# Kernel tuning notes

Measured on AMD Instinct MI355X. Metric: run time of the kernel, lower is better.

## Reference

```python
import jax, jax.numpy as jnp
import numpy as np

B, S, M, H, P, T = 32, 400, 400, 200, 16, 4

def setup_inputs() -> dict:
    key = jax.random.key(0)
    ks = jax.random.split(key, 20)
    sc = 0.05
    inp = {
        'att': jax.random.normal(ks[0], (B, S, M), jnp.float32),
        'mod': jax.random.normal(ks[1], (B, S, M), jnp.float32),
        'mask': jnp.ones((B, S), jnp.float32),
        # LSTMCell: input 2*M, hidden H, gate order i,f,g,o
        'lstm_Wih': jax.random.normal(ks[2], (4 * H, 2 * M), jnp.float32) * sc,
        'lstm_Whh': jax.random.normal(ks[3], (4 * H, H), jnp.float32) * sc,
        'lstm_bih': jnp.zeros((4 * H,), jnp.float32),
        'lstm_bhh': jnp.zeros((4 * H,), jnp.float32),
    }
    for pfx, off in (('s', 4), ('e', 11)):
        inp[pfx + '_rW'] = jax.random.normal(ks[off + 0], (H, 2 * M + H), jnp.float32) * sc
        inp[pfx + '_W1'] = jax.random.normal(ks[off + 1], (P * H, M + H), jnp.float32) * sc
        inp[pfx + '_b1'] = jnp.zeros((P * H,), jnp.float32)
        inp[pfx + '_W2'] = jax.random.normal(ks[off + 2], (P * H, H), jnp.float32) * sc
        inp[pfx + '_b2'] = jnp.zeros((P * H,), jnp.float32)
        inp[pfx + '_W3'] = jax.random.normal(ks[off + 3], (P, 2 * H), jnp.float32) * sc
        inp[pfx + '_b3'] = jnp.zeros((P,), jnp.float32)
    return inp

def _gather(mod, idx):
    # mod:[B,S,M], idx:[B] -> [B,M]
    return jnp.take_along_axis(mod, idx[:, None, None], axis=1)[:, 0, :]

def _lstm_cell(x, h, c, Wih, Whh, bih, bhh):
    g = x @ Wih.T + bih + h @ Whh.T + bhh  # [B,4H]
    i, f, gg, o = jnp.split(g, 4, axis=1)
    c2 = jax.nn.sigmoid(f) * c + jax.nn.sigmoid(i) * jnp.tanh(gg)
    h2 = jax.nn.sigmoid(o) * jnp.tanh(c2)
    return h2, c2

def _hmn(mod, h, us, ue, mask, rW, W1, b1, W2, b2, W3, b3):
    r = jnp.tanh(jnp.concatenate([h, us, ue], 1) @ rW.T)  # [B,H]
    x = jnp.concatenate([mod, jnp.broadcast_to(r[:, None, :], (B, S, H))], 2)  # [B,S,M+H]
    m1 = (x @ W1.T + b1).reshape(B, S, P, H).max(2)   # maxout 1
    m2 = (m1 @ W2.T + b2).reshape(B, S, P, H).max(2)  # maxout 2
    logits = (jnp.concatenate([m1, m2], 2) @ W3.T + b3).max(2)  # [B,S]
    logits = jnp.where(mask > 0, logits, -1e30)
    return jax.nn.log_softmax(logits, axis=1)

def reference(att, mod, mask, lstm_Wih, lstm_Whh, lstm_bih, lstm_bhh,
              s_rW, s_W1, s_b1, s_W2, s_b2, s_W3, s_b3,
              e_rW, e_W1, e_b1, e_W2, e_b2, e_W3, e_b3):
    s_prev = jnp.zeros((B,), jnp.int32)
    e_prev = jnp.sum(mask, 1).astype(jnp.int32) - 1
    h = jnp.zeros((B, H), mod.dtype)
    c = jnp.zeros((B, H), mod.dtype)
    log_p1s, log_p2s = [], []
    for _ in range(T):
        u_s = _gather(mod, s_prev)
        u_e = _gather(mod, e_prev)
        h, c = _lstm_cell(jnp.concatenate([u_s, u_e], 1), h, c,
                          lstm_Wih, lstm_Whh, lstm_bih, lstm_bhh)
        lp1 = _hmn(mod, h, u_s, u_e, mask, s_rW, s_W1, s_b1, s_W2, s_b2, s_W3, s_b3)
        s_prev = jnp.argmax(lp1, axis=1).astype(jnp.int32)
        u_s = _gather(mod, s_prev)
        lp2 = _hmn(mod, h, u_s, u_e, mask, e_rW, e_W1, e_b1, e_W2, e_b2, e_W3, e_b3)
        e_prev = jnp.argmax(lp2, axis=1).astype(jnp.int32)
        log_p1s.append(lp1)
        log_p2s.append(lp2)
    return jnp.stack(log_p1s, 1), jnp.stack(log_p2s, 1)  # each [B,T,S]
```

## Files before the change

kernel.cpp:

```cpp
#include <hip/hip_runtime.h>
#include <math.h>

#define NB 32
#define NS 400
#define NM 400
#define NH 200
#define NP 16
#define NT 4
#define NBS (NB*NS)
#define NPH (NP*NH)
#define NX  (2*NM)
#define NG  (4*NH)
#define NR  (2*NM+NH)
#define K1  1280
#define K2  640

typedef __attribute__((ext_vector_type(8))) short short8v;
typedef __attribute__((ext_vector_type(4))) float f32x4;
typedef __attribute__((ext_vector_type(4))) unsigned short us4;
typedef unsigned short ushort;

__device__ __forceinline__ float sigf(float x){ return 1.0f/(1.0f+expf(-x)); }

__device__ __forceinline__ ushort f2bf(float x){
  union{float f; unsigned u;} v; v.f=x;
  unsigned r = v.u + 0x7fffu + ((v.u>>16)&1u);
  return (ushort)(r>>16);
}
__device__ __forceinline__ float bf2f(ushort u){
  union{float f; unsigned v;} x; x.v = ((unsigned)u)<<16; return x.f;
}
__device__ __forceinline__ float wave_sum(float v){
  #pragma unroll
  for (int o=32;o>0;o>>=1) v += __shfl_xor(v, o);
  return v;
}

__global__ __launch_bounds__(256) void init_kernel(const float* __restrict__ mask,
    float* __restrict__ h, float* __restrict__ c,
    int* __restrict__ sprev, int* __restrict__ eprev){
  int b = blockIdx.x, tid = threadIdx.x;
  __shared__ float red[256];
  float s = 0.f;
  for (int i=tid;i<NS;i+=256) s += mask[(size_t)b*NS+i];
  red[tid]=s; __syncthreads();
  for (int st=128;st>0;st>>=1){ if(tid<st) red[tid]+=red[tid+st]; __syncthreads(); }
  if (tid==0){ sprev[b]=0; eprev[b]=(int)red[0]-1; }
  for (int i=tid;i<NH;i+=256){ h[(size_t)b*NH+i]=0.f; c[(size_t)b*NH+i]=0.f; }
}

__global__ __launch_bounds__(256) void conv_mod_k(const float* __restrict__ in, ushort* __restrict__ out){
  for (size_t i = (size_t)blockIdx.x*256+threadIdx.x; i < (size_t)NBS*NM; i += (size_t)gridDim.x*256){
    int r = (int)(i/NM), k = (int)(i%NM);
    float x = in[i];
    ushort h = f2bf(x); ushort lo = f2bf(x - bf2f(h));
    ushort* o = out + (size_t)r*K1;
    o[k]=h; o[NM+k]=lo; o[2*NM+k]=h;
  }
}
__global__ __launch_bounds__(256) void conv_w1_k(const float* __restrict__ in, ushort* __restrict__ out){
  for (size_t i = (size_t)blockIdx.x*256+threadIdx.x; i < (size_t)NPH*NM; i += (size_t)gridDim.x*256){
    int j = (int)(i/NM), k = (int)(i%NM);
    int jp = (j%NH)*NP + j/NH;
    float x = in[(size_t)j*(NM+NH)+k];
    ushort h = f2bf(x); ushort lo = f2bf(x - bf2f(h));
    ushort* o = out + (size_t)jp*K1;
    o[k]=h; o[NM+k]=h; o[2*NM+k]=lo;
  }
}
__global__ __launch_bounds__(256) void conv_w2_k(const float* __restrict__ in, ushort* __restrict__ out){
  for (size_t i = (size_t)blockIdx.x*256+threadIdx.x; i < (size_t)NPH*NH; i += (size_t)gridDim.x*256){
    int j = (int)(i/NH), k = (int)(i%NH);
    int jp = (j%NH)*NP + j/NH;
    float x = in[(size_t)j*NH+k];
    ushort h = f2bf(x); ushort lo = f2bf(x - bf2f(h));
    ushort* o = out + (size_t)jp*K2;
    o[k]=h; o[NH+k]=h; o[2*NH+k]=lo;
  }
}
__global__ __launch_bounds__(256) void conv_w1r_k(const float* __restrict__ in, float* __restrict__ out){
  for (size_t i = (size_t)blockIdx.x*256+threadIdx.x; i < (size_t)NH*NPH; i += (size_t)gridDim.x*256){
    int k = (int)(i/NPH), jp = (int)(i%NPH);
    int hh = jp>>4, p = jp&15, j = p*NH + hh;
    out[i] = in[(size_t)j*(NM+NH) + NM + k];
  }
}
__global__ __launch_bounds__(256) void permv_k(const float* __restrict__ in, float* __restrict__ out){
  int i = blockIdx.x*256+threadIdx.x;
  if (i < NPH) out[(i%NH)*NP + i/NH] = in[i];
}
__global__ __launch_bounds__(256) void pad_zero_k(ushort* __restrict__ p, int stride, int start, int width, int rows){
  for (size_t i = (size_t)blockIdx.x*256+threadIdx.x; i < (size_t)rows*width; i += (size_t)gridDim.x*256){
    int r = (int)(i/width), j = (int)(i%width);
    p[(size_t)r*stride + start + j] = 0;
  }
}

__global__ __launch_bounds__(256) void lstm_gates(const float* __restrict__ mod,
    const int* __restrict__ sprev, const int* __restrict__ eprev,
    const float* __restrict__ h,
    const float* __restrict__ Wih, const float* __restrict__ Whh,
    const float* __restrict__ bih, const float* __restrict__ bhh,
    float* __restrict__ gs){
  int b=blockIdx.x, tid=threadIdx.x;
  __shared__ float xs[NX+NH];
  const float* us = mod + ((size_t)b*NS + sprev[b])*NM;
  const float* ue = mod + ((size_t)b*NS + eprev[b])*NM;
  for (int i=tid;i<NM;i+=256){ xs[i]=us[i]; xs[NM+i]=ue[i]; }
  for (int i=tid;i<NH;i+=256) xs[NX+i]=h[(size_t)b*NH+i];
  __syncthreads();
  int w=tid>>6, lane=tid&63;
  int j = blockIdx.y*4 + w;
  const float* wih = Wih + (size_t)j*NX;
  const float* whh = Whh + (size_t)j*NH;
  float acc=0.f;
  for (int k=lane;k<NX;k+=64) acc += xs[k]*wih[k];
  for (int k=lane;k<NH;k+=64) acc += xs[NX+k]*whh[k];
  acc = wave_sum(acc);
  if (lane==0) gs[(size_t)b*NG+j] = acc + bih[j] + bhh[j];
}
__global__ __launch_bounds__(256) void lstm_update(const float* __restrict__ gs,
    float* __restrict__ h, float* __restrict__ c){
  int b=blockIdx.x, j=threadIdx.x;
  if (j<NH){
    float iv=gs[(size_t)b*NG+j], fv=gs[(size_t)b*NG+NH+j];
    float gv=gs[(size_t)b*NG+2*NH+j], ov=gs[(size_t)b*NG+3*NH+j];
    float c2 = sigf(fv)*c[(size_t)b*NH+j] + sigf(iv)*tanhf(gv);
    c[(size_t)b*NH+j]=c2;
    h[(size_t)b*NH+j]=sigf(ov)*tanhf(c2);
  }
}

__global__ __launch_bounds__(256) void r_kernel(const float* __restrict__ mod,
    const int* __restrict__ sprev, const int* __restrict__ eprev,
    const float* __restrict__ h, const float* __restrict__ rW,
    float* __restrict__ rbuf){
  int b=blockIdx.x, tid=threadIdx.x;
  __shared__ float zs[NR];
  const float* us = mod + ((size_t)b*NS + sprev[b])*NM;
  const float* ue = mod + ((size_t)b*NS + eprev[b])*NM;
  for (int i=tid;i<NH;i+=256) zs[i]=h[(size_t)b*NH+i];
  for (int i=tid;i<NM;i+=256){ zs[NH+i]=us[i]; zs[NH+NM+i]=ue[i]; }
  __syncthreads();
  int w=tid>>6, lane=tid&63;
  int j = blockIdx.y*4 + w;
  const float* wr = rW + (size_t)j*NR;
  float acc=0.f;
  for (int k=lane;k<NR;k+=64) acc += zs[k]*wr[k];
  acc = wave_sum(acc);
  if (lane==0) rbuf[(size_t)b*NH+j] = tanhf(acc);
}

__global__ __launch_bounds__(256) void prer_kernel(const float* __restrict__ rbuf,
    const float* __restrict__ W1rT, const float* __restrict__ b1p,
    float* __restrict__ prer){
  int b=blockIdx.x, tid=threadIdx.x;
  __shared__ float rs[NH];
  if (tid < NH) rs[tid] = rbuf[(size_t)b*NH+tid];
  __syncthreads();
  int jp = blockIdx.y*256 + tid;
  if (jp < NPH){
    float acc = b1p[jp];
    #pragma unroll 8
    for (int k=0;k<NH;k++) acc += rs[k]*W1rT[(size_t)k*NPH + jp];
    prer[(size_t)b*NPH + jp] = acc;
  }
}

template<int MODE>
__global__ __launch_bounds__(256) void gemm_fused(
    const ushort* __restrict__ A, const ushort* __restrict__ W, int ldk,
    const float* __restrict__ bias, void* __restrict__ outp){
  __shared__ __align__(16) ushort As[2][128*32];
  __shared__ __align__(16) ushort Bs[2][128*32];
  __shared__ float biasLds[2][128];
  __shared__ float outT[128][8];
  const int tid = threadIdx.x;
  const int i0 = blockIdx.x*128, j0 = blockIdx.y*128;
  const int b0 = i0/NS;
  if (MODE==0){
    if (tid<128) biasLds[0][tid] = bias[(size_t)b0*NPH + j0 + tid];
    else { int b1r = (i0+127)/NS; biasLds[1][tid-128] = bias[(size_t)b1r*NPH + j0 + (tid-128)]; }
  } else {
    if (tid<128) biasLds[0][tid] = bias[j0+tid];
  }
  const int l = tid&63, w = tid>>6;
  const int wr = w>>1, wc = w&1;
  const int srow = tid>>2, slot = tid&3;
  const int fr = l&15, fk = l>>4;
  const int ksteps = ldk>>5;
  auto stage = [&](int buf, int kt){
    #pragma unroll
    for (int r=0;r<2;r++){
      int row = r*64 + srow;
      int ss  = slot ^ ((row>>1)&3);
      const ushort* ga = A + (size_t)(i0+row)*ldk + kt*32 + ss*8;
      const ushort* gb = W + (size_t)(j0+row)*ldk + kt*32 + ss*8;
      __builtin_amdgcn_global_load_lds((const __attribute__((address_space(1))) void*)ga,
          (__attribute__((address_space(3))) void*)(&As[buf][row*32 + slot*8]), 16, 0, 0);
      __builtin_amdgcn_global_load_lds((const __attribute__((address_space(1))) void*)gb,
          (__attribute__((address_space(3))) void*)(&Bs[buf][row*32 + slot*8]), 16, 0, 0);
    }
  };
  f32x4 acc[4][4] = {};
  stage(0, 0);
  __syncthreads();
  int cur = 0;
  for (int kt=0; kt<ksteps; kt++){
    if (kt+1 < ksteps) stage(cur^1, kt+1);
    short8v af[4], bf[4];
    #pragma unroll
    for (int m=0;m<4;m++){
      int row = wr*64 + m*16 + fr;
      int sl = fk ^ ((row>>1)&3);
      af[m] = *(const short8v*)(&As[cur][row*32 + sl*8]);
    }
    #pragma unroll
    for (int n=0;n<4;n++){
      int row = wc*64 + n*16 + fr;
      int sl = fk ^ ((row>>1)&3);
      bf[n] = *(const short8v*)(&Bs[cur][row*32 + sl*8]);
    }
    #pragma unroll
    for (int m=0;m<4;m++)
      #pragma unroll
      for (int n=0;n<4;n++)
        acc[m][n] = __builtin_amdgcn_mfma_f32_16x16x32_bf16(af[m], bf[n], acc[m][n], 0,0,0);
    __syncthreads();
    cur ^= 1;
  }
  const int blim = (b0+1)*NS;
  #pragma unroll
  for (int m=0;m<4;m++){
    #pragma unroll
    for (int n=0;n<4;n++){
      int colL = wc*64 + n*16 + fr;
      int rbase = wr*64 + m*16 + fk*4;
      #pragma unroll
      for (int reg=0; reg<4; reg++){
        int rowL = rbase + reg;
        float bv;
        if (MODE==0) bv = ((i0+rowL) >= blim) ? biasLds[1][colL] : biasLds[0][colL];
        else bv = biasLds[0][colL];
        float v = acc[m][n][reg] + bv;
        v = fmaxf(v, __shfl_xor(v,1));
        v = fmaxf(v, __shfl_xor(v,2));
        v = fmaxf(v, __shfl_xor(v,4));
        v = fmaxf(v, __shfl_xor(v,8));
        if (fr==0) outT[rowL][wc*4+n] = v;
      }
    }
  }
  __syncthreads();
  {
    int rowL = tid>>1;
    int c4 = (tid&1)*4;
    int absrow = i0 + rowL;
    int hg0 = (j0>>4) + c4;
    float v0=outT[rowL][c4], v1=outT[rowL][c4+1], v2=outT[rowL][c4+2], v3=outT[rowL][c4+3];
    if (MODE==0){
      ushort* o = (ushort*)outp + (size_t)absrow*K2 + hg0;
      ushort h0=f2bf(v0), h1=f2bf(v1), h2=f2bf(v2), h3=f2bf(v3);
      ushort l0=f2bf(v0-bf2f(h0)), l1=f2bf(v1-bf2f(h1)), l2=f2bf(v2-bf2f(h2)), l3=f2bf(v3-bf2f(h3));
      *(us4*)(o)        = (us4){h0,h1,h2,h3};
      *(us4*)(o+NH)     = (us4){l0,l1,l2,l3};
      *(us4*)(o+2*NH)   = (us4){h0,h1,h2,h3};
    } else {
      float* o = (float*)outp + (size_t)absrow*NH + hg0;
      *(f32x4*)o = (f32x4){v0,v1,v2,v3};
    }
  }
}

__global__ __launch_bounds__(256) void logits_main(const ushort* __restrict__ m1e,
    const float* __restrict__ m2, const float* __restrict__ W3, const float* __restrict__ b3,
    const float* __restrict__ mask, float* __restrict__ lg){
  int b=blockIdx.x;
  int s=blockIdx.y*256+threadIdx.x;
  if (s >= NS) return;
  const ushort* a = m1e + (size_t)(b*NS+s)*K2;
  const float4* d = (const float4*)(m2 + (size_t)(b*NS+s)*NH);
  float acc[NP];
  #pragma unroll
  for (int p=0;p<NP;p++) acc[p]=b3[p];
  for (int k=0;k<NH/4;k++){
    us4 hv = *(const us4*)(a + 4*k);
    us4 lv = *(const us4*)(a + NH + 4*k);
    float4 dv = d[k];
    float a0=bf2f(hv.x)+bf2f(lv.x), a1=bf2f(hv.y)+bf2f(lv.y);
    float a2=bf2f(hv.z)+bf2f(lv.z), a3=bf2f(hv.w)+bf2f(lv.w);
    #pragma unroll
    for (int p=0;p<NP;p++){
      const float* wp = W3 + p*(2*NH) + 4*k;
      acc[p] += a0*wp[0]+a1*wp[1]+a2*wp[2]+a3*wp[3];
      const float* w2 = wp + NH;
      acc[p] += dv.x*w2[0]+dv.y*w2[1]+dv.z*w2[2]+dv.w*w2[3];
    }
  }
  float best=acc[0];
  #pragma unroll
  for (int p=1;p<NP;p++) best=fmaxf(best,acc[p]);
  lg[(size_t)b*NS+s] = (mask[(size_t)b*NS+s] > 0.f) ? best : -1e30f;
}

__global__ __launch_bounds__(256) void logits_fin(const float* __restrict__ lg,
    float* __restrict__ out, int t, int* __restrict__ prevIdx){
  int b=blockIdx.x, tid=threadIdx.x;
  __shared__ float rv[256]; __shared__ int ri[256]; __shared__ float sv[256];
  float bv=-INFINITY; int bi=NS;
  for (int s=tid;s<NS;s+=256){ float v=lg[(size_t)b*NS+s]; if (v>bv){bv=v;bi=s;} }
  rv[tid]=bv; ri[tid]=bi; __syncthreads();
  for (int st=128;st>0;st>>=1){
    if (tid<st){
      float v2=rv[tid+st]; int i2=ri[tid+st];
      if (v2>rv[tid] || (v2==rv[tid] && i2<ri[tid])){ rv[tid]=v2; ri[tid]=i2; }
    }
    __syncthreads();
  }
  float mx = rv[0];
  float ps=0.f;
  for (int s=tid;s<NS;s+=256) ps += expf(lg[(size_t)b*NS+s]-mx);
  sv[tid]=ps; __syncthreads();
  for (int st=128;st>0;st>>=1){ if (tid<st) sv[tid]+=sv[tid+st]; __syncthreads(); }
  float lse = mx + logf(sv[0]);
  for (int s=tid;s<NS;s+=256) out[((size_t)b*NT + t)*NS + s] = lg[(size_t)b*NS+s]-lse;
  if (tid==0) prevIdx[b]=ri[0];
}

extern "C" void kernel_launch(void* const* d_in, const int* in_sizes, int n_in,
                              void* d_out, int out_size, void* d_ws, size_t ws_size,
                              hipStream_t stream){
  const float* mod  = (const float*)d_in[1];
  const float* mask = (const float*)d_in[2];
  const float* Wih  = (const float*)d_in[3];
  const float* Whh  = (const float*)d_in[4];
  const float* bih  = (const float*)d_in[5];
  const float* bhh  = (const float*)d_in[6];
  const float* rW[2] = {(const float*)d_in[7],  (const float*)d_in[14]};
  const float* W1[2] = {(const float*)d_in[8],  (const float*)d_in[15]};
  const float* b1[2] = {(const float*)d_in[9],  (const float*)d_in[16]};
  const float* W2[2] = {(const float*)d_in[10], (const float*)d_in[17]};
  const float* b2[2] = {(const float*)d_in[11], (const float*)d_in[18]};
  const float* W3[2] = {(const float*)d_in[12], (const float*)d_in[19]};
  const float* b3[2] = {(const float*)d_in[13], (const float*)d_in[20]};
  float* out[2];
  out[0] = (float*)d_out;
  out[1] = out[0] + (size_t)NB*NT*NS;

  float* wsf = (float*)d_ws;
  size_t off = 0;
  auto carve = [&](size_t n)->size_t{ size_t o=off; off += (n + 63) & ~(size_t)63; return o; };
  float* hbuf   = wsf + carve((size_t)NB*NH);
  float* cbuf   = wsf + carve((size_t)NB*NH);
  float* prer   = wsf + carve((size_t)NB*NPH);
  int*   sprev  = (int*)(wsf + carve(128));
  int*   eprev  = sprev + 32;
  float* m2f    = wsf + carve((size_t)NBS*NH);
  float* b2p[2] = {wsf + carve(NPH), wsf + carve(NPH)};
  float* b1p[2] = {wsf + carve(NPH), wsf + carve(NPH)};
  float* rbuf   = wsf + carve((size_t)NB*NH);
  float* gsbuf  = wsf + carve((size_t)NB*NG);
  float* lgbuf  = wsf + carve((size_t)NB*NS);
  float* W1rT[2]= {wsf + carve((size_t)NH*NPH), wsf + carve((size_t)NH*NPH)};
  ushort* modExp   = (ushort*)(wsf + carve((size_t)NBS*K1/2));
  ushort* W1exp[2] = {(ushort*)(wsf + carve((size_t)NPH*K1/2)),
                      (ushort*)(wsf + carve((size_t)NPH*K1/2))};
  ushort* W2exp[2] = {(ushort*)(wsf + carve((size_t)NPH*K2/2)),
                      (ushort*)(wsf + carve((size_t)NPH*K2/2))};
  ushort* m1exp    = (ushort*)(wsf + carve((size_t)NBS*K2/2));

  init_kernel<<<NB, 256, 0, stream>>>(mask, hbuf, cbuf, sprev, eprev);
  conv_mod_k<<<2048, 256, 0, stream>>>(mod, modExp);
  pad_zero_k<<<256, 256, 0, stream>>>(modExp, K1, 3*NM, K1-3*NM, NBS);
  pad_zero_k<<<256, 256, 0, stream>>>(m1exp, K2, 3*NH, K2-3*NH, NBS);
  for (int net=0; net<2; net++){
    conv_w1_k<<<2048, 256, 0, stream>>>(W1[net], W1exp[net]);
    pad_zero_k<<<64, 256, 0, stream>>>(W1exp[net], K1, 3*NM, K1-3*NM, NPH);
    conv_w2_k<<<1024, 256, 0, stream>>>(W2[net], W2exp[net]);
    pad_zero_k<<<64, 256, 0, stream>>>(W2exp[net], K2, 3*NH, K2-3*NH, NPH);
    conv_w1r_k<<<1024, 256, 0, stream>>>(W1[net], W1rT[net]);
    permv_k<<<(NPH+255)/256, 256, 0, stream>>>(b2[net], b2p[net]);
    permv_k<<<(NPH+255)/256, 256, 0, stream>>>(b1[net], b1p[net]);
  }

  dim3 ggrid(NBS/128, NPH/128);
  for (int t=0; t<NT; t++){
    lstm_gates<<<dim3(NB, NG/4), 256, 0, stream>>>(mod, sprev, eprev, hbuf,
                                                   Wih, Whh, bih, bhh, gsbuf);
    lstm_update<<<NB, 256, 0, stream>>>(gsbuf, hbuf, cbuf);
    for (int net=0; net<2; net++){
      r_kernel<<<dim3(NB, NH/4), 256, 0, stream>>>(mod, sprev, eprev, hbuf, rW[net], rbuf);
      prer_kernel<<<dim3(NB, (NPH+255)/256), 256, 0, stream>>>(rbuf, W1rT[net], b1p[net], prer);
      gemm_fused<0><<<ggrid, 256, 0, stream>>>(modExp, W1exp[net], K1, prer, (void*)m1exp);
      gemm_fused<1><<<ggrid, 256, 0, stream>>>(m1exp, W2exp[net], K2, b2p[net], (void*)m2f);
      logits_main<<<dim3(NB, 2), 256, 0, stream>>>(m1exp, m2f, W3[net], b3[net], mask, lgbuf);
      logits_fin<<<NB, 256, 0, stream>>>(lgbuf, out[net], t, net==0 ? sprev : eprev);
    }
  }
}
```

Before: 3.124 ms.

## Enlarge GEMM tiles to 256x256 with 512 threads and deeper K pipeline

The fused maxout GEMMs move from 128x128 tiles with 256 threads and K-step 32 to 256x256 tiles with 512 threads and K-step 64. The prefetch runs two stages ahead, synchronised with explicit vmcnt waits and raw barriers, and the MFMA blocks are wrapped in setprio. The output dimension is padded from 3200 to 3328 so it divides by 256, and the weight, bias and prer buffers are zero-filled in the padding. The conversion kernels now write their zero padding directly, which removes the separate pad kernels. Larger tiles raise operand reuse and cut global traffic, but they use more LDS and registers and pay for the padded columns.

```diff
diff --git a/kernel.cpp b/kernel.cpp
--- a/kernel.cpp
+++ b/kernel.cpp
@@ -9,6 +9,7 @@
 #define NT 4
 #define NBS (NB*NS)
 #define NPH (NP*NH)
+#define NPH2 3328
 #define NX  (2*NM)
 #define NG  (4*NH)
 #define NR  (2*NM+NH)
@@ -50,32 +51,41 @@
 }
 
 __global__ __launch_bounds__(256) void conv_mod_k(const float* __restrict__ in, ushort* __restrict__ out){
-  for (size_t i = (size_t)blockIdx.x*256+threadIdx.x; i < (size_t)NBS*NM; i += (size_t)gridDim.x*256){
-    int r = (int)(i/NM), k = (int)(i%NM);
-    float x = in[i];
-    ushort h = f2bf(x); ushort lo = f2bf(x - bf2f(h));
-    ushort* o = out + (size_t)r*K1;
-    o[k]=h; o[NM+k]=lo; o[2*NM+k]=h;
+  for (size_t i = (size_t)blockIdx.x*256+threadIdx.x; i < (size_t)NBS*K1; i += (size_t)gridDim.x*256){
+    int r = (int)(i/K1), k = (int)(i%K1);
+    ushort v = 0;
+    if (k < 3*NM){
+      float x = in[(size_t)r*NM + (k % NM)];
+      ushort h = f2bf(x);
+      v = (k < NM || k >= 2*NM) ? h : f2bf(x - bf2f(h));
+    }
+    out[i] = v;
   }
 }
 __global__ __launch_bounds__(256) void conv_w1_k(const float* __restrict__ in, ushort* __restrict__ out){
-  for (size_t i = (size_t)blockIdx.x*256+threadIdx.x; i < (size_t)NPH*NM; i += (size_t)gridDim.x*256){
-    int j = (int)(i/NM), k = (int)(i%NM);
-    int jp = (j%NH)*NP + j/NH;
-    float x = in[(size_t)j*(NM+NH)+k];
-    ushort h = f2bf(x); ushort lo = f2bf(x - bf2f(h));
-    ushort* o = out + (size_t)jp*K1;
-    o[k]=h; o[NM+k]=h; o[2*NM+k]=lo;
+  for (size_t i = (size_t)blockIdx.x*256+threadIdx.x; i < (size_t)NPH2*K1; i += (size_t)gridDim.x*256){
+    int jp = (int)(i/K1), k = (int)(i%K1);
+    ushort v = 0;
+    if (jp < NPH && k < 3*NM){
+      int j = (jp&15)*NH + (jp>>4);
+      float x = in[(size_t)j*(NM+NH) + (k % NM)];
+      ushort h = f2bf(x);
+      v = (k < 2*NM) ? h : f2bf(x - bf2f(h));
+    }
+    out[i] = v;
   }
 }
 __global__ __launch_bounds__(256) void conv_w2_k(const float* __restrict__ in, ushort* __restrict__ out){
-  for (size_t i = (size_t)blockIdx.x*256+threadIdx.x; i < (size_t)NPH*NH; i += (size_t)gridDim.x*256){
-    int j = (int)(i/NH), k = (int)(i%NH);
-    int jp = (j%NH)*NP + j/NH;
-    float x = in[(size_t)j*NH+k];
-    ushort h = f2bf(x); ushort lo = f2bf(x - bf2f(h));
-    ushort* o = out + (size_t)jp*K2;
-    o[k]=h; o[NH+k]=h; o[2*NH+k]=lo;
+  for (size_t i = (size_t)blockIdx.x*256+threadIdx.x; i < (size_t)NPH2*K2; i += (size_t)gridDim.x*256){
+    int jp = (int)(i/K2), k = (int)(i%K2);
+    ushort v = 0;
+    if (jp < NPH && k < 3*NH){
+      int j = (jp&15)*NH + (jp>>4);
+      float x = in[(size_t)j*NH + (k % NH)];
+      ushort h = f2bf(x);
+      v = (k < 2*NH) ? h : f2bf(x - bf2f(h));
+    }
+    out[i] = v;
   }
 }
 __global__ __launch_bounds__(256) void conv_w1r_k(const float* __restrict__ in, float* __restrict__ out){
@@ -88,6 +98,7 @@
 __global__ __launch_bounds__(256) void permv_k(const float* __restrict__ in, float* __restrict__ out){
   int i = blockIdx.x*256+threadIdx.x;
   if (i < NPH) out[(i%NH)*NP + i/NH] = in[i];
+  else if (i < NPH2) out[i] = 0.f;
 }
 __global__ __launch_bounds__(256) void pad_zero_k(ushort* __restrict__ p, int stride, int start, int width, int rows){
   for (size_t i = (size_t)blockIdx.x*256+threadIdx.x; i < (size_t)rows*width; i += (size_t)gridDim.x*256){
@@ -159,89 +170,96 @@
   if (tid < NH) rs[tid] = rbuf[(size_t)b*NH+tid];
   __syncthreads();
   int jp = blockIdx.y*256 + tid;
-  if (jp < NPH){
-    float acc = b1p[jp];
-    #pragma unroll 8
-    for (int k=0;k<NH;k++) acc += rs[k]*W1rT[(size_t)k*NPH + jp];
-    prer[(size_t)b*NPH + jp] = acc;
+  if (jp < NPH2){
+    float acc = 0.f;
+    if (jp < NPH){
+      acc = b1p[jp];
+      #pragma unroll 8
+      for (int k=0;k<NH;k++) acc += rs[k]*W1rT[(size_t)k*NPH + jp];
+    }
+    prer[(size_t)b*NPH2 + jp] = acc;
   }
 }
 
 template<int MODE>
-__global__ __launch_bounds__(256) void gemm_fused(
-    const ushort* __restrict__ A, const ushort* __restrict__ W, int ldk,
+__global__ __launch_bounds__(512, 2) void gemm_fused(
+    const ushort* __restrict__ A, const ushort* __restrict__ W,
     const float* __restrict__ bias, void* __restrict__ outp){
-  __shared__ __align__(16) ushort As[2][128*32];
-  __shared__ __align__(16) ushort Bs[2][128*32];
-  __shared__ float biasLds[2][128];
-  __shared__ float outT[128][8];
+  constexpr int LDK = (MODE==0) ? K1 : K2;
+  constexpr int NTI = LDK/64;
+  __shared__ __align__(16) ushort As[2][256*64];
+  __shared__ __align__(16) ushort Bs[2][256*64];
+  __shared__ float biasLds[2][256];
+  __shared__ float outT[256][16];
   const int tid = threadIdx.x;
-  const int i0 = blockIdx.x*128, j0 = blockIdx.y*128;
+  const int i0 = blockIdx.x*256, j0 = blockIdx.y*256;
   const int b0 = i0/NS;
   if (MODE==0){
-    if (tid<128) biasLds[0][tid] = bias[(size_t)b0*NPH + j0 + tid];
-    else { int b1r = (i0+127)/NS; biasLds[1][tid-128] = bias[(size_t)b1r*NPH + j0 + (tid-128)]; }
+    if (tid<256) biasLds[0][tid] = bias[(size_t)b0*NPH2 + j0 + tid];
+    else { int b1r=(i0+255)/NS; biasLds[1][tid-256] = bias[(size_t)b1r*NPH2 + j0 + (tid-256)]; }
   } else {
-    if (tid<128) biasLds[0][tid] = bias[j0+tid];
-  }
-  const int l = tid&63, w = tid>>6;
-  const int wr = w>>1, wc = w&1;
-  const int srow = tid>>2, slot = tid&3;
+    if (tid<256) biasLds[0][tid] = bias[j0+tid];
+  }
+  const int w = tid>>6, l = tid&63;
+  const int wr = w>>2, wc = w&3;
   const int fr = l&15, fk = l>>4;
-  const int ksteps = ldk>>5;
-  auto stage = [&](int buf, int kt){
+  const int swz = ((l&7) ^ (l>>3))*8;
+  const ushort* gA = A + (size_t)(i0 + w*32 + (l>>3))*LDK + swz;
+  const ushort* gB = W + (size_t)(j0 + w*32 + (l>>3))*LDK + swz;
+  const int wOff = w*2048 + l*8;
+  auto stage = [&](int slot, int kt){
+    const ushort* a0 = gA + kt*64;
+    const ushort* b0g = gB + kt*64;
     #pragma unroll
-    for (int r=0;r<2;r++){
-      int row = r*64 + srow;
-      int ss  = slot ^ ((row>>1)&3);
-      const ushort* ga = A + (size_t)(i0+row)*ldk + kt*32 + ss*8;
-      const ushort* gb = W + (size_t)(j0+row)*ldk + kt*32 + ss*8;
-      __builtin_amdgcn_global_load_lds((const __attribute__((address_space(1))) void*)ga,
-          (__attribute__((address_space(3))) void*)(&As[buf][row*32 + slot*8]), 16, 0, 0);
-      __builtin_amdgcn_global_load_lds((const __attribute__((address_space(1))) void*)gb,
-          (__attribute__((address_space(3))) void*)(&Bs[buf][row*32 + slot*8]), 16, 0, 0);
-    }
+    for (int j=0;j<4;j++)
+      __builtin_amdgcn_global_load_lds((const __attribute__((address_space(1))) void*)(a0 + (size_t)j*8*LDK),
+          (__attribute__((address_space(3))) void*)(&As[slot][wOff + j*512]), 16, 0, 0);
+    #pragma unroll
+    for (int j=0;j<4;j++)
+      __builtin_amdgcn_global_load_lds((const __attribute__((address_space(1))) void*)(b0g + (size_t)j*8*LDK),
+          (__attribute__((address_space(3))) void*)(&Bs[slot][wOff + j*512]), 16, 0, 0);
   };
-  f32x4 acc[4][4] = {};
+  f32x4 acc[8][4] = {};
   stage(0, 0);
+  stage(1, 1);
+  const int koffA = (fr&7)<<3;
+  for (int t=0; t<NTI; t++){
+    const int s = t&1;
+    if (t+1 < NTI) asm volatile("s_waitcnt vmcnt(8)" ::: "memory");
+    else           asm volatile("s_waitcnt vmcnt(0)" ::: "memory");
+    __builtin_amdgcn_s_barrier();
+    #pragma unroll
+    for (int ks=0; ks<2; ks++){
+      const int ko = (ks*32 + fk*8) ^ koffA;
+      short8v a[8], b[4];
+      #pragma unroll
+      for (int m=0;m<8;m++) a[m] = *(const short8v*)&As[s][(wr*128 + m*16 + fr)*64 + ko];
+      #pragma unroll
+      for (int n=0;n<4;n++) b[n] = *(const short8v*)&Bs[s][(wc*64 + n*16 + fr)*64 + ko];
+      __builtin_amdgcn_s_setprio(1);
+      #pragma unroll
+      for (int m=0;m<8;m++)
+        #pragma unroll
+        for (int n=0;n<4;n++)
+          acc[m][n] = __builtin_amdgcn_mfma_f32_16x16x32_bf16(a[m], b[n], acc[m][n], 0,0,0);
+      __builtin_amdgcn_s_setprio(0);
+    }
+    asm volatile("s_waitcnt lgkmcnt(0)" ::: "memory");
+    __builtin_amdgcn_s_barrier();
+    if (t+2 < NTI) stage(s, t+2);
+  }
   __syncthreads();
-  int cur = 0;
-  for (int kt=0; kt<ksteps; kt++){
-    if (kt+1 < ksteps) stage(cur^1, kt+1);
-    short8v af[4], bf[4];
-    #pragma unroll
-    for (int m=0;m<4;m++){
-      int row = wr*64 + m*16 + fr;
-      int sl = fk ^ ((row>>1)&3);
-      af[m] = *(const short8v*)(&As[cur][row*32 + sl*8]);
-    }
-    #pragma unroll
-    for (int n=0;n<4;n++){
-      int row = wc*64 + n*16 + fr;
-      int sl = fk ^ ((row>>1)&3);
-      bf[n] = *(const short8v*)(&Bs[cur][row*32 + sl*8]);
-    }
-    #pragma unroll
-    for (int m=0;m<4;m++)
-      #pragma unroll
-      for (int n=0;n<4;n++)
-        acc[m][n] = __builtin_amdgcn_mfma_f32_16x16x32_bf16(af[m], bf[n], acc[m][n], 0,0,0);
-    __syncthreads();
-    cur ^= 1;
-  }
   const int blim = (b0+1)*NS;
   #pragma unroll
-  for (int m=0;m<4;m++){
+  for (int m=0;m<8;m++){
     #pragma unroll
     for (int n=0;n<4;n++){
       int colL = wc*64 + n*16 + fr;
-      int rbase = wr*64 + m*16 + fk*4;
+      int rbase = wr*128 + m*16 + fk*4;
       #pragma unroll
       for (int reg=0; reg<4; reg++){
         int rowL = rbase + reg;
-        float bv;
-        if (MODE==0) bv = ((i0+rowL) >= blim) ? biasLds[1][colL] : biasLds[0][colL];
-        else bv = biasLds[0][colL];
+        float bv = (MODE==0 && (i0+rowL) >= blim) ? biasLds[1][colL] : biasLds[0][colL];
         float v = acc[m][n][reg] + bv;
         v = fmaxf(v, __shfl_xor(v,1));
         v = fmaxf(v, __shfl_xor(v,2));
@@ -254,20 +272,29 @@
   __syncthreads();
   {
     int rowL = tid>>1;
-    int c4 = (tid&1)*4;
-    int absrow = i0 + rowL;
-    int hg0 = (j0>>4) + c4;
-    float v0=outT[rowL][c4], v1=outT[rowL][c4+1], v2=outT[rowL][c4+2], v3=outT[rowL][c4+3];
-    if (MODE==0){
-      ushort* o = (ushort*)outp + (size_t)absrow*K2 + hg0;
-      ushort h0=f2bf(v0), h1=f2bf(v1), h2=f2bf(v2), h3=f2bf(v3);
-      ushort l0=f2bf(v0-bf2f(h0)), l1=f2bf(v1-bf2f(h1)), l2=f2bf(v2-bf2f(h2)), l3=f2bf(v3-bf2f(h3));
-      *(us4*)(o)        = (us4){h0,h1,h2,h3};
-      *(us4*)(o+NH)     = (us4){l0,l1,l2,l3};
-      *(us4*)(o+2*NH)   = (us4){h0,h1,h2,h3};
-    } else {
-      float* o = (float*)outp + (size_t)absrow*NH + hg0;
-      *(f32x4*)o = (f32x4){v0,v1,v2,v3};
+    int hloc0 = (tid&1)*8;
+    int hg0 = (j0>>4) + hloc0;
+    if (hg0 < NH){
+      int absrow = i0 + rowL;
+      float v[8];
+      #pragma unroll
+      for (int q=0;q<8;q++) v[q] = outT[rowL][hloc0+q];
+      if (MODE==0){
+        ushort* o = (ushort*)outp + (size_t)absrow*K2 + hg0;
+        ushort hi[8], lo[8];
+        #pragma unroll
+        for (int q=0;q<8;q++){ hi[q]=f2bf(v[q]); lo[q]=f2bf(v[q]-bf2f(hi[q])); }
+        *(us4*)(o)        = (us4){hi[0],hi[1],hi[2],hi[3]};
+        *(us4*)(o+4)      = (us4){hi[4],hi[5],hi[6],hi[7]};
+        *(us4*)(o+NH)     = (us4){lo[0],lo[1],lo[2],lo[3]};
+        *(us4*)(o+NH+4)   = (us4){lo[4],lo[5],lo[6],lo[7]};
+        *(us4*)(o+2*NH)   = (us4){hi[0],hi[1],hi[2],hi[3]};
+        *(us4*)(o+2*NH+4) = (us4){hi[4],hi[5],hi[6],hi[7]};
+      } else {
+        float* o = (float*)outp + (size_t)absrow*NH + hg0;
+        *(f32x4*)o     = (f32x4){v[0],v[1],v[2],v[3]};
+        *(f32x4*)(o+4) = (f32x4){v[4],v[5],v[6],v[7]};
+      }
     }
   }
 }
@@ -352,47 +379,44 @@
   auto carve = [&](size_t n)->size_t{ size_t o=off; off += (n + 63) & ~(size_t)63; return o; };
   float* hbuf   = wsf + carve((size_t)NB*NH);
   float* cbuf   = wsf + carve((size_t)NB*NH);
-  float* prer   = wsf + carve((size_t)NB*NPH);
+  float* prer   = wsf + carve((size_t)NB*NPH2);
   int*   sprev  = (int*)(wsf + carve(128));
   int*   eprev  = sprev + 32;
   float* m2f    = wsf + carve((size_t)NBS*NH);
-  float* b2p[2] = {wsf + carve(NPH), wsf + carve(NPH)};
-  float* b1p[2] = {wsf + carve(NPH), wsf + carve(NPH)};
+  float* b2p[2] = {wsf + carve(NPH2), wsf + carve(NPH2)};
+  float* b1p[2] = {wsf + carve(NPH2), wsf + carve(NPH2)};
   float* rbuf   = wsf + carve((size_t)NB*NH);
   float* gsbuf  = wsf + carve((size_t)NB*NG);
   float* lgbuf  = wsf + carve((size_t)NB*NS);
   float* W1rT[2]= {wsf + carve((size_t)NH*NPH), wsf + carve((size_t)NH*NPH)};
   ushort* modExp   = (ushort*)(wsf + carve((size_t)NBS*K1/2));
-  ushort* W1exp[2] = {(ushort*)(wsf + carve((size_t)NPH*K1/2)),
-                      (ushort*)(wsf + carve((size_t)NPH*K1/2))};
-  ushort* W2exp[2] = {(ushort*)(wsf + carve((size_t)NPH*K2/2)),
-                      (ushort*)(wsf + carve((size_t)NPH*K2/2))};
+  ushort* W1exp[2] = {(ushort*)(wsf + carve((size_t)NPH2*K1/2)),
+                      (ushort*)(wsf + carve((size_t)NPH2*K1/2))};
+  ushort* W2exp[2] = {(ushort*)(wsf + carve((size_t)NPH2*K2/2)),
+                      (ushort*)(wsf + carve((size_t)NPH2*K2/2))};
   ushort* m1exp    = (ushort*)(wsf + carve((size_t)NBS*K2/2));
 
   init_kernel<<<NB, 256, 0, stream>>>(mask, hbuf, cbuf, sprev, eprev);
   conv_mod_k<<<2048, 256, 0, stream>>>(mod, modExp);
-  pad_zero_k<<<256, 256, 0, stream>>>(modExp, K1, 3*NM, K1-3*NM, NBS);
   pad_zero_k<<<256, 256, 0, stream>>>(m1exp, K2, 3*NH, K2-3*NH, NBS);
   for (int net=0; net<2; net++){
     conv_w1_k<<<2048, 256, 0, stream>>>(W1[net], W1exp[net]);
-    pad_zero_k<<<64, 256, 0, stream>>>(W1exp[net], K1, 3*NM, K1-3*NM, NPH);
     conv_w2_k<<<1024, 256, 0, stream>>>(W2[net], W2exp[net]);
-    pad_zero_k<<<64, 256, 0, stream>>>(W2exp[net], K2, 3*NH, K2-3*NH, NPH);
     conv_w1r_k<<<1024, 256, 0, stream>>>(W1[net], W1rT[net]);
-    permv_k<<<(NPH+255)/256, 256, 0, stream>>>(b2[net], b2p[net]);
-    permv_k<<<(NPH+255)/256, 256, 0, stream>>>(b1[net], b1p[net]);
-  }
-
-  dim3 ggrid(NBS/128, NPH/128);
+    permv_k<<<(NPH2+255)/256, 256, 0, stream>>>(b2[net], b2p[net]);
+    permv_k<<<(NPH2+255)/256, 256, 0, stream>>>(b1[net], b1p[net]);
+  }
+
+  dim3 ggrid(NBS/256, NPH2/256);
   for (int t=0; t<NT; t++){
     lstm_gates<<<dim3(NB, NG/4), 256, 0, stream>>>(mod, sprev, eprev, hbuf,
                                                    Wih, Whh, bih, bhh, gsbuf);
     lstm_update<<<NB, 256, 0, stream>>>(gsbuf, hbuf, cbuf);
     for (int net=0; net<2; net++){
       r_kernel<<<dim3(NB, NH/4), 256, 0, stream>>>(mod, sprev, eprev, hbuf, rW[net], rbuf);
-      prer_kernel<<<dim3(NB, (NPH+255)/256), 256, 0, stream>>>(rbuf, W1rT[net], b1p[net], prer);
-      gemm_fused<0><<<ggrid, 256, 0, stream>>>(modExp, W1exp[net], K1, prer, (void*)m1exp);
-      gemm_fused<1><<<ggrid, 256, 0, stream>>>(m1exp, W2exp[net], K2, b2p[net], (void*)m2f);
+      prer_kernel<<<dim3(NB, NPH2/256), 256, 0, stream>>>(rbuf, W1rT[net], b1p[net], prer);
+      gemm_fused<0><<<ggrid, 512, 0, stream>>>(modExp, W1exp[net], prer, (void*)m1exp);
+      gemm_fused<1><<<ggrid, 512, 0, stream>>>(m1exp, W2exp[net], b2p[net], (void*)m2f);
       logits_main<<<dim3(NB, 2), 256, 0, stream>>>(m1exp, m2f, W3[net], b3[net], mask, lgbuf);
       logits_fin<<<NB, 256, 0, stream>>>(lgbuf, out[net], t, net==0 ? sprev : eprev);
     }
```

New measurement: 3.332 ms. 6.6% more time.
